# Optimization experiments

Hardware: AMD Instinct MI355X
Metric: run time of the kernel (lower is better)

The kernel has to match this reference:

```python
import jax, jax.numpy as jnp
import numpy as np

B, F0, D = 2048, 40, 32
LAYER0, LAYER1 = 128, 128  # layer_size=(128,128), split_half=True -> field_nums=[40,64]


def setup_inputs() -> dict:
    key = jax.random.key(0)
    k1, k2, k3 = jax.random.split(key, 3)
    x = jax.random.normal(k1, (B, F0, D), dtype=jnp.float32)
    # TF conv1d filters: [1, F_prev*F0, size]; we store them reshaped [F0, F_prev_fields, size]
    # Layer 0: F_prev = F0 = 40 -> W0 flattened index m = i*F0 + j, i over x0 fields, j over hidden fields
    W0 = jax.random.normal(k2, (F0, F0, LAYER0), dtype=jnp.float32) * 0.05
    b0 = jnp.zeros((LAYER0,), dtype=jnp.float32)
    # Layer 1: F_prev = LAYER0 // 2 = 64 (split_half)
    W1 = jax.random.normal(k3, (F0, LAYER0 // 2, LAYER1), dtype=jnp.float32) * 0.05
    b1 = jnp.zeros((LAYER1,), dtype=jnp.float32)
    return {"x": x, "W0": W0, "b0": b0, "W1": W1, "b1": b1}


def reference(x, W0, b0, W1, b1):
    # CIN layer 0: outer product x0 (x) x0 over fields per embedding dim, then 1x1 conv + bias + relu
    # TF flattens dot_result as index i*F_prev + j, matching W0[i, j, s].
    h0 = jax.nn.relu(jnp.einsum('bid,bjd,ijs->bsd', x, x, W0) + b0[None, :, None])  # (B, 128, D)
    half = LAYER0 // 2
    next_hidden, direct0 = h0[:, :half, :], h0[:, half:, :]  # split_half
    # CIN layer 1 (last layer): all feature maps go to direct connect
    direct1 = jax.nn.relu(
        jnp.einsum('bid,bjd,ijs->bsd', x, next_hidden, W1) + b1[None, :, None]
    )  # (B, 128, D)
    result = jnp.concatenate([direct0, direct1], axis=1)  # (B, 192, D)
    return jnp.sum(result, axis=-1)  # (B, 192)
```

## Files before the change

### kernel.cpp

```cpp
#include <hip/hip_runtime.h>
#include <stdint.h>


typedef __attribute__((ext_vector_type(8))) _Float16 half8;
typedef __attribute__((ext_vector_type(2))) _Float16 half2v;
typedef __attribute__((ext_vector_type(4))) float f32x4;

#define T0 30
#define T1 80
#define WBUF 20480

__host__ __device__ constexpr int ic0_of(int t) {
    return (t < 2) ? t : (t < 6) ? (t - 2) : (t < 12) ? (t - 6)
         : (t < 20) ? (t - 12) : (t - 20);
}
__host__ __device__ constexpr int jc0_of(int t) {
    return (t < 2) ? 0 : (t < 6) ? 1 : (t < 12) ? 2 : (t < 20) ? 3 : 4;
}

__device__ __forceinline__ unsigned short f2h(float f) {
    return __builtin_bit_cast(unsigned short, (_Float16)f);
}
__device__ __forceinline__ float qsum(float v) {
    v += __shfl_xor(v, 16, 64);
    v += __shfl_xor(v, 32, 64);
    return v;
}
__device__ __forceinline__ void gl_lds16(const unsigned short* g, unsigned short* l) {
    __builtin_amdgcn_global_load_lds(
        (const __attribute__((address_space(1))) unsigned int*)g,
        (__attribute__((address_space(3))) unsigned int*)l,
        16, 0, 0);
}

__global__ void permute_w_both(const float* __restrict__ W0, const float* __restrict__ W1,
                               unsigned short* __restrict__ Wp0, unsigned short* __restrict__ Wp1)
{
    const int t = blockIdx.x;
    const int tid = threadIdx.x;
    unsigned short outv[16];
    unsigned short* dst;
    if (t < T0) {
        const int ic = ic0_of(t), jc = jc0_of(t);
        #pragma unroll
        for (int q = 0; q < 16; ++q) {
            int pos  = tid * 16 + q;
            int oc   = pos & 7, lane = (pos >> 3) & 63;
            int nt   = (pos >> 9) & 3, sh = pos >> 11;
            int s    = sh * 64 + nt * 16 + (lane & 15);
            int i    = ic * 4 + (lane >> 4), j = jc * 8 + oc;
            float v = 0.0f;
            if (i < j)       v = W0[((size_t)(i * 40 + j)) * 128 + s]
                               + W0[((size_t)(j * 40 + i)) * 128 + s];
            else if (i == j) v = W0[((size_t)(i * 40 + i)) * 128 + s];
            outv[q] = f2h(v);
        }
        dst = Wp0 + (size_t)t * 4096 + tid * 16;
    } else {
        const int tt = t - T0;
        const int jc = tt / 10, ic = tt % 10;
        #pragma unroll
        for (int q = 0; q < 16; ++q) {
            int pos  = tid * 16 + q;
            int oc   = pos & 7, lane = (pos >> 3) & 63;
            int nt   = (pos >> 9) & 3, sh = pos >> 11;
            int s    = sh * 64 + nt * 16 + (lane & 15);
            int i    = ic * 4 + (lane >> 4), j = jc * 8 + oc;
            outv[q] = f2h(W1[((size_t)(i * 64 + j)) * 128 + s]);
        }
        dst = Wp1 + (size_t)tt * 4096 + tid * 16;
    }
    *(uint4*)dst       = *(const uint4*)outv;
    *(uint4*)(dst + 8) = *(const uint4*)(outv + 8);
}

template<int T, int PHASE>
__device__ __forceinline__ void gemm_phase(
    const unsigned short* __restrict__ Wp,
    const unsigned short* __restrict__ Jl,
    int jstride,
    const unsigned int xi2[4][10],
    unsigned short* Wb,
    f32x4 acc[4][4], int tid)
{
    const int lane = tid & 63;
    const int wv = tid >> 6;
    const int rt = wv & 3;
    const int sh = tid >> 8;
    const int ml = lane & 15;

    const unsigned short* jrow[4];
    #pragma unroll
    for (int mt = 0; mt < 4; ++mt)
        jrow[mt] = Jl + (rt * 64 + mt * 16 + ml) * jstride;

    const unsigned short* brd = Wb + sh * 2048 + lane * 8;
    const unsigned short* gsrc = Wp + tid * 8;
    unsigned short* ldst = Wb + wv * 512;

    auto stage_period = [&](int buf, int t0) {
        #pragma unroll
        for (int u = 0; u < 5; ++u)
            gl_lds16(gsrc + (size_t)(t0 + u) * 4096, ldst + buf * WBUF + u * 4096);
    };

    stage_period(0, 0);
    __syncthreads();

    uint4 jv[4];
    constexpr int NP = T / 5;
    #pragma unroll
    for (int p = 0; p < NP; ++p) {
        const int cb = p & 1;
        const int nb = cb ^ 1;
        if ((p + 1) * 5 < T) stage_period(nb, (p + 1) * 5);
        #pragma unroll
        for (int u = 0; u < 5; ++u) {
            const int t  = p * 5 + u;
            const int ic = (PHASE == 0) ? ic0_of(t) : (t % 10);
            const int jc = (PHASE == 0) ? jc0_of(t) : (t / 10);
            const bool rl = (t == 0) ||
                (jc != ((PHASE == 0) ? jc0_of(t - 1) : ((t - 1) / 10)));
            if (rl) {
                #pragma unroll
                for (int mt = 0; mt < 4; ++mt)
                    jv[mt] = *(const uint4*)(jrow[mt] + jc * 8);
            }
            uint4 bv[4];
            #pragma unroll
            for (int nt = 0; nt < 4; ++nt)
                bv[nt] = *(const uint4*)(brd + cb * WBUF + u * 4096 + nt * 512);
            uint4 av[4];
            #pragma unroll
            for (int mt = 0; mt < 4; ++mt) {
                half2v x2 = __builtin_bit_cast(half2v, xi2[mt][ic]);
                av[mt].x = __builtin_bit_cast(unsigned int,
                    (half2v)(x2 * __builtin_bit_cast(half2v, jv[mt].x)));
                av[mt].y = __builtin_bit_cast(unsigned int,
                    (half2v)(x2 * __builtin_bit_cast(half2v, jv[mt].y)));
                av[mt].z = __builtin_bit_cast(unsigned int,
                    (half2v)(x2 * __builtin_bit_cast(half2v, jv[mt].z)));
                av[mt].w = __builtin_bit_cast(unsigned int,
                    (half2v)(x2 * __builtin_bit_cast(half2v, jv[mt].w)));
            }
            #pragma unroll
            for (int mt = 0; mt < 4; ++mt)
                #pragma unroll
                for (int nt = 0; nt < 4; ++nt)
                    acc[mt][nt] = __builtin_amdgcn_mfma_f32_16x16x32_f16(
                        __builtin_bit_cast(half8, av[mt]),
                        __builtin_bit_cast(half8, bv[nt]),
                        acc[mt][nt], 0, 0, 0);
        }
        __syncthreads();
    }
}

__global__ __launch_bounds__(512, 2)
void fused_two_layer(const float* __restrict__ x,
                     const unsigned short* __restrict__ W0p,
                     const float* __restrict__ b0,
                     const unsigned short* __restrict__ W1p,
                     const float* __restrict__ b1,
                     float* __restrict__ out)
{
    __shared__ __align__(16) unsigned short Xl[256 * 40];
    __shared__ __align__(16) unsigned short NH[256 * 72];
    __shared__ __align__(16) unsigned short Wb[2 * WBUF];

    const int tid  = threadIdx.x;
    const int lane = tid & 63;
    const int rt   = (tid >> 6) & 3;
    const int sh   = tid >> 8;
    const int ml   = lane & 15;
    const int kc   = lane >> 4;

    const float* xblk = x + (size_t)blockIdx.x * (8 * 40 * 32);
    #pragma unroll
    for (int bl = 0; bl < 8; ++bl) {
        #pragma unroll
        for (int k = 0; k < 3; ++k) {
            int f = 512 * k + tid;
            if (f < 1280) {
                int i = f >> 5, d = f & 31;
                Xl[(bl * 32 + d) * 40 + i] = f2h(xblk[bl * 1280 + f]);
            }
        }
    }
    __syncthreads();

    unsigned int xi2[4][10];
    #pragma unroll
    for (int mt = 0; mt < 4; ++mt) {
        const unsigned short* xr = Xl + (rt * 64 + mt * 16 + ml) * 40;
        #pragma unroll
        for (int ic = 0; ic < 10; ++ic) {
            unsigned int u = xr[ic * 4 + kc];
            xi2[mt][ic] = u | (u << 16);
        }
    }

    f32x4 acc[4][4];
    const f32x4 zero4 = {0.f, 0.f, 0.f, 0.f};
    #pragma unroll
    for (int mt = 0; mt < 4; ++mt)
        #pragma unroll
        for (int nt = 0; nt < 4; ++nt) acc[mt][nt] = zero4;

    gemm_phase<T0, 0>(W0p, Xl, 40, xi2, Wb, acc, tid);

    {
        float bias[4];
        #pragma unroll
        for (int nt = 0; nt < 4; ++nt) bias[nt] = b0[sh * 64 + nt * 16 + ml];
        if (sh == 0) {
            #pragma unroll
            for (int mt = 0; mt < 4; ++mt) {
                int r = rt * 64 + mt * 16 + (kc << 2);
                #pragma unroll
                for (int nt = 0; nt < 4; ++nt) {
                    int s = nt * 16 + ml;
                    #pragma unroll
                    for (int rg = 0; rg < 4; ++rg) {
                        float v = fmaxf(acc[mt][nt][rg] + bias[nt], 0.0f);
                        NH[(r + rg) * 72 + s] = f2h(v);
                    }
                }
            }
        } else {
            int bb = blockIdx.x * 8 + rt * 2;
            #pragma unroll
            for (int nt = 0; nt < 4; ++nt) {
                float sA = 0.f, sB = 0.f;
                #pragma unroll
                for (int rg = 0; rg < 4; ++rg) {
                    sA += fmaxf(acc[0][nt][rg] + bias[nt], 0.f) + fmaxf(acc[1][nt][rg] + bias[nt], 0.f);
                    sB += fmaxf(acc[2][nt][rg] + bias[nt], 0.f) + fmaxf(acc[3][nt][rg] + bias[nt], 0.f);
                }
                sA = qsum(sA); sB = qsum(sB);
                if (lane < 16) {
                    int col = nt * 16 + lane;
                    out[(size_t)bb * 192 + col]       = sA;
                    out[(size_t)(bb + 1) * 192 + col] = sB;
                }
            }
        }
    }
    __syncthreads();

    #pragma unroll
    for (int mt = 0; mt < 4; ++mt)
        #pragma unroll
        for (int nt = 0; nt < 4; ++nt) acc[mt][nt] = zero4;

    gemm_phase<T1, 1>(W1p, NH, 72, xi2, Wb, acc, tid);

    {
        float bias[4];
        #pragma unroll
        for (int nt = 0; nt < 4; ++nt) bias[nt] = b1[sh * 64 + nt * 16 + ml];
        int bb = blockIdx.x * 8 + rt * 2;
        #pragma unroll
        for (int nt = 0; nt < 4; ++nt) {
            float sA = 0.f, sB = 0.f;
            #pragma unroll
            for (int rg = 0; rg < 4; ++rg) {
                sA += fmaxf(acc[0][nt][rg] + bias[nt], 0.f) + fmaxf(acc[1][nt][rg] + bias[nt], 0.f);
                sB += fmaxf(acc[2][nt][rg] + bias[nt], 0.f) + fmaxf(acc[3][nt][rg] + bias[nt], 0.f);
            }
            sA = qsum(sA); sB = qsum(sB);
            if (lane < 16) {
                int col = 64 + sh * 64 + nt * 16 + lane;
                out[(size_t)bb * 192 + col]       = sA;
                out[(size_t)(bb + 1) * 192 + col] = sB;
            }
        }
    }
}

extern "C" void kernel_launch(void* const* d_in, const int* in_sizes, int n_in,
                              void* d_out, int out_size, void* d_ws, size_t ws_size,
                              hipStream_t stream) {
    const float* x  = (const float*)d_in[0];
    const float* W0 = (const float*)d_in[1];
    const float* b0 = (const float*)d_in[2];
    const float* W1 = (const float*)d_in[3];
    const float* b1 = (const float*)d_in[4];
    float* out = (float*)d_out;

    unsigned short* W0p = (unsigned short*)d_ws;
    unsigned short* W1p = (unsigned short*)((char*)d_ws + T0 * 4096 * 2);

    permute_w_both<<<T0 + T1, 256, 0, stream>>>(W0, W1, W0p, W1p);
    fused_two_layer<<<256, 512, 0, stream>>>(x, W0p, b0, W1p, b1, out);
}
```

Before: 117.7 us.

## Halve rows per block, double grid, and shrink weight staging period

Each block now handles 4 batch rows (128 GEMM rows) instead of 8, so the grid doubles to 512 blocks with smaller per-thread accumulators (2x4 tiles). Weight tiles are staged in periods of 3 instead of 5, which shrinks LDS double buffers; phase 1 is padded to 81 tiles with a zero tile and zeroed NH padding columns. This aims to spread work over more CUs and raise occupancy (launch bounds 4 blocks), at the cost of each block streaming the full weight set, doubling total weight traffic from L2, and of more barriers per block.

New measurement: 116.8 us. No clear change (-0.8%).

```diff
diff --git a/kernel.cpp b/kernel.cpp
--- a/kernel.cpp
+++ b/kernel.cpp
@@ -7,8 +7,9 @@
 typedef __attribute__((ext_vector_type(4))) float f32x4;
 
 #define T0 30
-#define T1 80
-#define WBUF 20480
+#define T1P 81
+#define PERIOD 3
+#define WBUF 12288
 
 __host__ __device__ constexpr int ic0_of(int t) {
     return (t < 2) ? t : (t < 6) ? (t - 2) : (t < 12) ? (t - 6)
@@ -58,15 +59,20 @@
         dst = Wp0 + (size_t)t * 4096 + tid * 16;
     } else {
         const int tt = t - T0;
-        const int jc = tt / 10, ic = tt % 10;
-        #pragma unroll
-        for (int q = 0; q < 16; ++q) {
-            int pos  = tid * 16 + q;
-            int oc   = pos & 7, lane = (pos >> 3) & 63;
-            int nt   = (pos >> 9) & 3, sh = pos >> 11;
-            int s    = sh * 64 + nt * 16 + (lane & 15);
-            int i    = ic * 4 + (lane >> 4), j = jc * 8 + oc;
-            outv[q] = f2h(W1[((size_t)(i * 64 + j)) * 128 + s]);
+        if (tt == 80) {
+            #pragma unroll
+            for (int q = 0; q < 16; ++q) outv[q] = 0;
+        } else {
+            const int jc = tt / 10, ic = tt % 10;
+            #pragma unroll
+            for (int q = 0; q < 16; ++q) {
+                int pos  = tid * 16 + q;
+                int oc   = pos & 7, lane = (pos >> 3) & 63;
+                int nt   = (pos >> 9) & 3, sh = pos >> 11;
+                int s    = sh * 64 + nt * 16 + (lane & 15);
+                int i    = ic * 4 + (lane >> 4), j = jc * 8 + oc;
+                outv[q] = f2h(W1[((size_t)(i * 64 + j)) * 128 + s]);
+            }
         }
         dst = Wp1 + (size_t)tt * 4096 + tid * 16;
     }
@@ -79,20 +85,20 @@
     const unsigned short* __restrict__ Wp,
     const unsigned short* __restrict__ Jl,
     int jstride,
-    const unsigned int xi2[4][10],
+    const unsigned int xi2[2][10],
     unsigned short* Wb,
-    f32x4 acc[4][4], int tid)
+    f32x4 acc[2][4], int tid)
 {
     const int lane = tid & 63;
     const int wv = tid >> 6;
     const int rt = wv & 3;
-    const int sh = tid >> 8;
+    const int sh = wv >> 2;
     const int ml = lane & 15;
 
-    const unsigned short* jrow[4];
-    #pragma unroll
-    for (int mt = 0; mt < 4; ++mt)
-        jrow[mt] = Jl + (rt * 64 + mt * 16 + ml) * jstride;
+    const unsigned short* jrow[2];
+    #pragma unroll
+    for (int mt = 0; mt < 2; ++mt)
+        jrow[mt] = Jl + (rt * 32 + mt * 16 + ml) * jstride;
 
     const unsigned short* brd = Wb + sh * 2048 + lane * 8;
     const unsigned short* gsrc = Wp + tid * 8;
@@ -100,39 +106,39 @@
 
     auto stage_period = [&](int buf, int t0) {
         #pragma unroll
-        for (int u = 0; u < 5; ++u)
+        for (int u = 0; u < PERIOD; ++u)
             gl_lds16(gsrc + (size_t)(t0 + u) * 4096, ldst + buf * WBUF + u * 4096);
     };
 
     stage_period(0, 0);
     __syncthreads();
 
-    uint4 jv[4];
-    constexpr int NP = T / 5;
+    uint4 jv[2];
+    constexpr int NP = T / PERIOD;
     #pragma unroll
     for (int p = 0; p < NP; ++p) {
         const int cb = p & 1;
         const int nb = cb ^ 1;
-        if ((p + 1) * 5 < T) stage_period(nb, (p + 1) * 5);
-        #pragma unroll
-        for (int u = 0; u < 5; ++u) {
-            const int t  = p * 5 + u;
+        if ((p + 1) * PERIOD < T) stage_period(nb, (p + 1) * PERIOD);
+        #pragma unroll
+        for (int u = 0; u < PERIOD; ++u) {
+            const int t  = p * PERIOD + u;
             const int ic = (PHASE == 0) ? ic0_of(t) : (t % 10);
             const int jc = (PHASE == 0) ? jc0_of(t) : (t / 10);
             const bool rl = (t == 0) ||
                 (jc != ((PHASE == 0) ? jc0_of(t - 1) : ((t - 1) / 10)));
             if (rl) {
                 #pragma unroll
-                for (int mt = 0; mt < 4; ++mt)
+                for (int mt = 0; mt < 2; ++mt)
                     jv[mt] = *(const uint4*)(jrow[mt] + jc * 8);
             }
             uint4 bv[4];
             #pragma unroll
             for (int nt = 0; nt < 4; ++nt)
                 bv[nt] = *(const uint4*)(brd + cb * WBUF + u * 4096 + nt * 512);
-            uint4 av[4];
-            #pragma unroll
-            for (int mt = 0; mt < 4; ++mt) {
+            uint4 av[2];
+            #pragma unroll
+            for (int mt = 0; mt < 2; ++mt) {
                 half2v x2 = __builtin_bit_cast(half2v, xi2[mt][ic]);
                 av[mt].x = __builtin_bit_cast(unsigned int,
                     (half2v)(x2 * __builtin_bit_cast(half2v, jv[mt].x)));
@@ -144,7 +150,7 @@
                     (half2v)(x2 * __builtin_bit_cast(half2v, jv[mt].w)));
             }
             #pragma unroll
-            for (int mt = 0; mt < 4; ++mt)
+            for (int mt = 0; mt < 2; ++mt)
                 #pragma unroll
                 for (int nt = 0; nt < 4; ++nt)
                     acc[mt][nt] = __builtin_amdgcn_mfma_f32_16x16x32_f16(
@@ -156,7 +162,7 @@
     }
 }
 
-__global__ __launch_bounds__(512, 2)
+__global__ __launch_bounds__(512, 4)
 void fused_two_layer(const float* __restrict__ x,
                      const unsigned short* __restrict__ W0p,
                      const float* __restrict__ b0,
@@ -164,35 +170,32 @@
                      const float* __restrict__ b1,
                      float* __restrict__ out)
 {
-    __shared__ __align__(16) unsigned short Xl[256 * 40];
-    __shared__ __align__(16) unsigned short NH[256 * 72];
+    __shared__ __align__(16) unsigned short Xl[128 * 40];
+    __shared__ __align__(16) unsigned short NH[128 * 72];
     __shared__ __align__(16) unsigned short Wb[2 * WBUF];
 
     const int tid  = threadIdx.x;
     const int lane = tid & 63;
-    const int rt   = (tid >> 6) & 3;
-    const int sh   = tid >> 8;
+    const int wv   = tid >> 6;
+    const int rt   = wv & 3;
+    const int sh   = wv >> 2;
     const int ml   = lane & 15;
     const int kc   = lane >> 4;
 
-    const float* xblk = x + (size_t)blockIdx.x * (8 * 40 * 32);
-    #pragma unroll
-    for (int bl = 0; bl < 8; ++bl) {
-        #pragma unroll
-        for (int k = 0; k < 3; ++k) {
-            int f = 512 * k + tid;
-            if (f < 1280) {
-                int i = f >> 5, d = f & 31;
-                Xl[(bl * 32 + d) * 40 + i] = f2h(xblk[bl * 1280 + f]);
-            }
-        }
+    const float* xblk = x + (size_t)blockIdx.x * (4 * 40 * 32);
+    #pragma unroll
+    for (int k = 0; k < 10; ++k) {
+        int f = 512 * k + tid;
+        int bl = f / 1280, rem = f - bl * 1280;
+        int i = rem >> 5, d = rem & 31;
+        Xl[(bl * 32 + d) * 40 + i] = f2h(xblk[f]);
     }
     __syncthreads();
 
-    unsigned int xi2[4][10];
-    #pragma unroll
-    for (int mt = 0; mt < 4; ++mt) {
-        const unsigned short* xr = Xl + (rt * 64 + mt * 16 + ml) * 40;
+    unsigned int xi2[2][10];
+    #pragma unroll
+    for (int mt = 0; mt < 2; ++mt) {
+        const unsigned short* xr = Xl + (rt * 32 + mt * 16 + ml) * 40;
         #pragma unroll
         for (int ic = 0; ic < 10; ++ic) {
             unsigned int u = xr[ic * 4 + kc];
@@ -200,10 +203,10 @@
         }
     }
 
-    f32x4 acc[4][4];
+    f32x4 acc[2][4];
     const f32x4 zero4 = {0.f, 0.f, 0.f, 0.f};
     #pragma unroll
-    for (int mt = 0; mt < 4; ++mt)
+    for (int mt = 0; mt < 2; ++mt)
         #pragma unroll
         for (int nt = 0; nt < 4; ++nt) acc[mt][nt] = zero4;
 
@@ -215,8 +218,8 @@
         for (int nt = 0; nt < 4; ++nt) bias[nt] = b0[sh * 64 + nt * 16 + ml];
         if (sh == 0) {
             #pragma unroll
-            for (int mt = 0; mt < 4; ++mt) {
-                int r = rt * 64 + mt * 16 + (kc << 2);
+            for (int mt = 0; mt < 2; ++mt) {
+                int r = rt * 32 + mt * 16 + (kc << 2);
                 #pragma unroll
                 for (int nt = 0; nt < 4; ++nt) {
                     int s = nt * 16 + ml;
@@ -227,53 +230,51 @@
                     }
                 }
             }
+            {
+                int rp = rt * 32 + (lane >> 1);
+                int a  = rp * 72 + 64 + (lane & 1) * 4;
+                *(unsigned int*)&NH[a]     = 0u;
+                *(unsigned int*)&NH[a + 2] = 0u;
+            }
         } else {
-            int bb = blockIdx.x * 8 + rt * 2;
+            int bb = blockIdx.x * 4 + rt;
             #pragma unroll
             for (int nt = 0; nt < 4; ++nt) {
-                float sA = 0.f, sB = 0.f;
-                #pragma unroll
-                for (int rg = 0; rg < 4; ++rg) {
-                    sA += fmaxf(acc[0][nt][rg] + bias[nt], 0.f) + fmaxf(acc[1][nt][rg] + bias[nt], 0.f);
-                    sB += fmaxf(acc[2][nt][rg] + bias[nt], 0.f) + fmaxf(acc[3][nt][rg] + bias[nt], 0.f);
-                }
-                sA = qsum(sA); sB = qsum(sB);
-                if (lane < 16) {
-                    int col = nt * 16 + lane;
-                    out[(size_t)bb * 192 + col]       = sA;
-                    out[(size_t)(bb + 1) * 192 + col] = sB;
-                }
+                float sA = 0.f;
+                #pragma unroll
+                for (int rg = 0; rg < 4; ++rg)
+                    sA += fmaxf(acc[0][nt][rg] + bias[nt], 0.f)
+                        + fmaxf(acc[1][nt][rg] + bias[nt], 0.f);
+                sA = qsum(sA);
+                if (lane < 16)
+                    out[(size_t)bb * 192 + nt * 16 + lane] = sA;
             }
         }
     }
     __syncthreads();
 
     #pragma unroll
-    for (int mt = 0; mt < 4; ++mt)
+    for (int mt = 0; mt < 2; ++mt)
         #pragma unroll
         for (int nt = 0; nt < 4; ++nt) acc[mt][nt] = zero4;
 
-    gemm_phase<T1, 1>(W1p, NH, 72, xi2, Wb, acc, tid);
+    gemm_phase<T1P, 1>(W1p, NH, 72, xi2, Wb, acc, tid);
 
     {
         float bias[4];
         #pragma unroll
         for (int nt = 0; nt < 4; ++nt) bias[nt] = b1[sh * 64 + nt * 16 + ml];
-        int bb = blockIdx.x * 8 + rt * 2;
+        int bb = blockIdx.x * 4 + rt;
         #pragma unroll
         for (int nt = 0; nt < 4; ++nt) {
-            float sA = 0.f, sB = 0.f;
-            #pragma unroll
-            for (int rg = 0; rg < 4; ++rg) {
-                sA += fmaxf(acc[0][nt][rg] + bias[nt], 0.f) + fmaxf(acc[1][nt][rg] + bias[nt], 0.f);
-                sB += fmaxf(acc[2][nt][rg] + bias[nt], 0.f) + fmaxf(acc[3][nt][rg] + bias[nt], 0.f);
-            }
-            sA = qsum(sA); sB = qsum(sB);
-            if (lane < 16) {
-                int col = 64 + sh * 64 + nt * 16 + lane;
-                out[(size_t)bb * 192 + col]       = sA;
-                out[(size_t)(bb + 1) * 192 + col] = sB;
-            }
+            float sA = 0.f;
+            #pragma unroll
+            for (int rg = 0; rg < 4; ++rg)
+                sA += fmaxf(acc[0][nt][rg] + bias[nt], 0.f)
+                    + fmaxf(acc[1][nt][rg] + bias[nt], 0.f);
+            sA = qsum(sA);
+            if (lane < 16)
+                out[(size_t)bb * 192 + 64 + sh * 64 + nt * 16 + lane] = sA;
         }
     }
 }
@@ -291,6 +292,6 @@
     unsigned short* W0p = (unsigned short*)d_ws;
     unsigned short* W1p = (unsigned short*)((char*)d_ws + T0 * 4096 * 2);
 
-    permute_w_both<<<T0 + T1, 256, 0, stream>>>(W0, W1, W0p, W1p);
-    fused_two_layer<<<256, 512, 0, stream>>>(x, W0p, b0, W1p, b1, out);
-}
+    permute_w_both<<<T0 + T1P, 256, 0, stream>>>(W0, W1, W0p, W1p);
+    fused_two_layer<<<512, 512, 0, stream>>>(x, W0p, b0, W1p, b1, out);
+}
```
